# Kernel tuning notes

Hardware: AMD Instinct MI355X
Metric: run time of the kernel (lower is better)

## Reference

```python
import jax, jax.numpy as jnp
import numpy as np

D_MODEL = 256
NUM_HEADS = 4
HEAD_DIM = D_MODEL // NUM_HEADS


def setup_inputs() -> dict:
    key = jax.random.key(0)
    ks = jax.random.split(key, 16)
    B, N, M, C = 2, 256, 256, D_MODEL
    inp = {
        'q_tokens': jax.random.normal(ks[0], (B, N, C), jnp.float32),
        'k_tokens': jax.random.normal(ks[1], (B, M, C), jnp.float32),
        'v_tokens': jax.random.normal(ks[2], (B, M, C), jnp.float32),
        'qk_embeds': jax.random.normal(ks[3], (B, N, M, C), jnp.float32),
        'qv_embeds': jax.random.normal(ks[4], (B, N, M, C), jnp.float32),
    }
    scale = 1.0 / np.sqrt(C)
    # Linear layer params (weight used as x @ W + b)
    inp['Wq'] = jax.random.normal(ks[5], (C, C), jnp.float32) * scale
    inp['bq'] = jnp.zeros((C,), jnp.float32)
    inp['Wk'] = jax.random.normal(ks[6], (C, C), jnp.float32) * scale
    inp['bk'] = jnp.zeros((C,), jnp.float32)
    inp['Wv'] = jax.random.normal(ks[7], (C, C), jnp.float32) * scale
    inp['bv'] = jnp.zeros((C,), jnp.float32)
    inp['Wqk'] = jax.random.normal(ks[8], (C, C), jnp.float32) * scale
    inp['bqk'] = jnp.zeros((C,), jnp.float32)
    inp['Wqv'] = jax.random.normal(ks[9], (C, C), jnp.float32) * scale
    inp['bqv'] = jnp.zeros((C,), jnp.float32)
    return inp


def reference(q_tokens, k_tokens, v_tokens, qk_embeds, qv_embeds,
              Wq, bq, Wk, bk, Wv, bv, Wqk, bqk, Wqv, bqv):
    B, N, C = q_tokens.shape
    M = k_tokens.shape[1]
    H, hc = NUM_HEADS, HEAD_DIM

    # token projections -> (B, H, len, hc)
    q = (q_tokens @ Wq + bq).reshape(B, N, H, hc).transpose(0, 2, 1, 3)
    k = (k_tokens @ Wk + bk).reshape(B, M, H, hc).transpose(0, 2, 1, 3)
    v = (v_tokens @ Wv + bv).reshape(B, M, H, hc).transpose(0, 2, 1, 3)

    # pair-embedding projections -> (B, N, M, H, hc)
    qk = (qk_embeds @ Wqk + bqk).reshape(B, N, M, H, hc)
    qv = (qv_embeds @ Wqv + bqv).reshape(B, N, M, H, hc)

    # scores: q . (k + qk)  == q.k + q.qk
    scores = jnp.einsum('bhnc,bhmc->bhnm', q, k)
    scores = scores + jnp.einsum('bhnc,bnmhc->bhnm', q, qk)
    scores = scores / np.sqrt(hc).astype(np.float32)

    attn = jax.nn.softmax(scores, axis=-1)  # (B, H, N, M)

    # output: attn @ (v + qv) == attn@v + attn.qv
    hidden = jnp.einsum('bhnm,bhmc->bhnc', attn, v)
    hidden = hidden + jnp.einsum('bhnm,bnmhc->bhnc', attn, qv)
    hidden = hidden.transpose(0, 2, 1, 3).reshape(B, N, C)  # (B, N, C)
    return hidden, attn
```

## Files before the change

kernel.cpp:

```cpp
#include <hip/hip_runtime.h>

#define BB 2
#define NN 256
#define CC 256

__device__ __forceinline__ float dot4acc(float4 e, float4 w, float s) {
    s = fmaf(e.x, w.x, s); s = fmaf(e.y, w.y, s);
    s = fmaf(e.z, w.z, s); s = fmaf(e.w, w.w, s);
    return s;
}

__global__ __launch_bounds__(256) void proj_gemm(
    const float* __restrict__ q_tok, const float* __restrict__ k_tok, const float* __restrict__ v_tok,
    const float* __restrict__ Wq, const float* __restrict__ bq,
    const float* __restrict__ Wk, const float* __restrict__ bk,
    const float* __restrict__ Wv, const float* __restrict__ bv,
    float* __restrict__ out)
{
    const int row0 = blockIdx.x * 64;
    const int col0 = blockIdx.y * 64;
    const int seg  = row0 >> 9;
    const float* A    = seg == 0 ? q_tok : (seg == 1 ? k_tok : v_tok);
    const float* W    = seg == 0 ? Wq    : (seg == 1 ? Wk    : Wv);
    const float* bias = seg == 0 ? bq    : (seg == 1 ? bk    : bv);
    const int ar0 = row0 & 511;

    __shared__ float As[64][17];
    __shared__ float Bs[16][68];
    const int t  = threadIdx.x;
    const int tr = t >> 4, tc = t & 15;
    float acc[4][4] = {};

    const int sr  = t >> 2, sk4 = (t & 3) << 2;
    const int bkr = t >> 4, bj4 = (t & 15) << 2;

    for (int k0 = 0; k0 < 256; k0 += 16) {
        float4 a4 = *reinterpret_cast<const float4*>(&A[(ar0 + sr) * 256 + k0 + sk4]);
        float4 b4 = *reinterpret_cast<const float4*>(&W[(k0 + bkr) * 256 + col0 + bj4]);
        As[sr][sk4 + 0] = a4.x; As[sr][sk4 + 1] = a4.y; As[sr][sk4 + 2] = a4.z; As[sr][sk4 + 3] = a4.w;
        Bs[bkr][bj4 + 0] = b4.x; Bs[bkr][bj4 + 1] = b4.y; Bs[bkr][bj4 + 2] = b4.z; Bs[bkr][bj4 + 3] = b4.w;
        __syncthreads();
        #pragma unroll
        for (int k = 0; k < 16; ++k) {
            float a[4], bbv[4];
            #pragma unroll
            for (int i = 0; i < 4; ++i) a[i] = As[tr * 4 + i][k];
            #pragma unroll
            for (int j = 0; j < 4; ++j) bbv[j] = Bs[k][tc * 4 + j];
            #pragma unroll
            for (int i = 0; i < 4; ++i)
                #pragma unroll
                for (int j = 0; j < 4; ++j)
                    acc[i][j] = fmaf(a[i], bbv[j], acc[i][j]);
        }
        __syncthreads();
    }
    #pragma unroll
    for (int i = 0; i < 4; ++i) {
        const int r = row0 + tr * 4 + i;
        #pragma unroll
        for (int j = 0; j < 4; ++j) {
            const int cj = col0 + tc * 4 + j;
            out[r * 256 + cj] = acc[i][j] + bias[cj];
        }
    }
}

__global__ __launch_bounds__(256) void qw_gemm(
    const float* __restrict__ qp, const float* __restrict__ Wqk, float* __restrict__ qW)
{
    const int h    = blockIdx.z;
    const int row0 = blockIdx.x * 64;
    const int d0   = blockIdx.y * 64;
    __shared__ float As[64][17];
    __shared__ float Bs[16][68];
    const int t  = threadIdx.x;
    const int tr = t >> 4, tc = t & 15;
    float acc[4][4] = {};
    const int sr = t >> 2, sc4 = (t & 3) << 2;

    for (int k0 = 0; k0 < 64; k0 += 16) {
        float4 a4 = *reinterpret_cast<const float4*>(&qp[(row0 + sr) * 256 + h * 64 + k0 + sc4]);
        float4 b4 = *reinterpret_cast<const float4*>(&Wqk[(d0 + sr) * 256 + h * 64 + k0 + sc4]);
        As[sr][sc4 + 0] = a4.x; As[sr][sc4 + 1] = a4.y; As[sr][sc4 + 2] = a4.z; As[sr][sc4 + 3] = a4.w;
        Bs[sc4 + 0][sr] = b4.x; Bs[sc4 + 1][sr] = b4.y; Bs[sc4 + 2][sr] = b4.z; Bs[sc4 + 3][sr] = b4.w;
        __syncthreads();
        #pragma unroll
        for (int k = 0; k < 16; ++k) {
            float a[4], bbv[4];
            #pragma unroll
            for (int i = 0; i < 4; ++i) a[i] = As[tr * 4 + i][k];
            #pragma unroll
            for (int j = 0; j < 4; ++j) bbv[j] = Bs[k][tc * 4 + j];
            #pragma unroll
            for (int i = 0; i < 4; ++i)
                #pragma unroll
                for (int j = 0; j < 4; ++j)
                    acc[i][j] = fmaf(a[i], bbv[j], acc[i][j]);
        }
        __syncthreads();
    }
    #pragma unroll
    for (int i = 0; i < 4; ++i)
        #pragma unroll
        for (int j = 0; j < 4; ++j)
            qW[((row0 + tr * 4 + i) * 4 + h) * 256 + d0 + tc * 4 + j] = acc[i][j];
}

__global__ __launch_bounds__(256) void qk_gemm(
    const float* __restrict__ qkvp, float* __restrict__ Sqk)
{
    const int bh = blockIdx.z;
    const int b  = bh >> 2, h = bh & 3;
    const int n0 = blockIdx.x * 64;
    const int m0 = blockIdx.y * 64;
    __shared__ float As[64][17];
    __shared__ float Bs[16][68];
    const int t  = threadIdx.x;
    const int tr = t >> 4, tc = t & 15;
    float acc[4][4] = {};
    const int sr = t >> 2, sc4 = (t & 3) << 2;

    for (int k0 = 0; k0 < 64; k0 += 16) {
        float4 a4 = *reinterpret_cast<const float4*>(&qkvp[(size_t)(b * 256 + n0 + sr) * 256 + h * 64 + k0 + sc4]);
        float4 b4 = *reinterpret_cast<const float4*>(&qkvp[(size_t)(512 + b * 256 + m0 + sr) * 256 + h * 64 + k0 + sc4]);
        As[sr][sc4 + 0] = a4.x; As[sr][sc4 + 1] = a4.y; As[sr][sc4 + 2] = a4.z; As[sr][sc4 + 3] = a4.w;
        Bs[sc4 + 0][sr] = b4.x; Bs[sc4 + 1][sr] = b4.y; Bs[sc4 + 2][sr] = b4.z; Bs[sc4 + 3][sr] = b4.w;
        __syncthreads();
        #pragma unroll
        for (int k = 0; k < 16; ++k) {
            float a[4], bbv[4];
            #pragma unroll
            for (int i = 0; i < 4; ++i) a[i] = As[tr * 4 + i][k];
            #pragma unroll
            for (int j = 0; j < 4; ++j) bbv[j] = Bs[k][tc * 4 + j];
            #pragma unroll
            for (int i = 0; i < 4; ++i)
                #pragma unroll
                for (int j = 0; j < 4; ++j)
                    acc[i][j] = fmaf(a[i], bbv[j], acc[i][j]);
        }
        __syncthreads();
    }
    #pragma unroll
    for (int i = 0; i < 4; ++i)
        #pragma unroll
        for (int j = 0; j < 4; ++j)
            Sqk[(size_t)((b * 4 + h) * 256 + n0 + tr * 4 + i) * 256 + m0 + tc * 4 + j] = acc[i][j];
}

__global__ __launch_bounds__(512, 4) void mega3(
    const float* __restrict__ qk_emb, const float* __restrict__ qv_emb,
    const float* __restrict__ qkvp, const float* __restrict__ qW,
    const float* __restrict__ Sqk, const float* __restrict__ Wqv,
    const float* __restrict__ bqv,
    float* __restrict__ attn_out, float* __restrict__ hidden)
{
    const int bn = blockIdx.x;
    const int b  = bn >> 8, n = bn & 255;
    const int t  = threadIdx.x;
    const int w  = t >> 6, l = t & 63;

    __shared__ float qWs[1024];
    __shared__ float SqkL[1024];
    __shared__ float Ssc[1024];
    __shared__ float attn_s[1024];
    __shared__ float Ap[4096];
    __shared__ float stage[16][256];
    __shared__ float pr[2][256];
    __shared__ float mxs[8][4], sums[8][4], scl[8][4];

    if (t < 256)
        *reinterpret_cast<float4*>(&qWs[t * 4]) =
            *reinterpret_cast<const float4*>(&qW[(size_t)bn * 1024 + t * 4]);
    __syncthreads();

    const int lq = l & 15, lr = l >> 4, li = l & 31;

    if (l < 32) {
        #pragma unroll
        for (int h = 0; h < 4; ++h)
            SqkL[h * 256 + w * 32 + li] =
                Sqk[(size_t)((b * 4 + h) * 256 + n) * 256 + w * 32 + li];
    }

    #pragma unroll
    for (int g = 0; g < 8; g += 2) {
        const int m0 = w * 32 + g * 4 + lr;
        const float* r0 = qk_emb + (size_t)(bn * 256 + m0) * 256 + lq * 4;
        const float* r1 = r0 + 1024;
        const float4 e00 = *reinterpret_cast<const float4*>(r0);
        const float4 e01 = *reinterpret_cast<const float4*>(r0 + 64);
        const float4 e02 = *reinterpret_cast<const float4*>(r0 + 128);
        const float4 e03 = *reinterpret_cast<const float4*>(r0 + 192);
        const float4 e10 = *reinterpret_cast<const float4*>(r1);
        const float4 e11 = *reinterpret_cast<const float4*>(r1 + 64);
        const float4 e12 = *reinterpret_cast<const float4*>(r1 + 128);
        const float4 e13 = *reinterpret_cast<const float4*>(r1 + 192);
        float p0[4], p1[4];
        #pragma unroll
        for (int hh = 0; hh < 4; ++hh) {
            const float4 w0 = *reinterpret_cast<const float4*>(&qWs[hh * 256 + lq * 4]);
            const float4 w1 = *reinterpret_cast<const float4*>(&qWs[hh * 256 + 64 + lq * 4]);
            const float4 w2 = *reinterpret_cast<const float4*>(&qWs[hh * 256 + 128 + lq * 4]);
            const float4 w3 = *reinterpret_cast<const float4*>(&qWs[hh * 256 + 192 + lq * 4]);
            float s0 = 0.f, s1 = 0.f;
            s0 = dot4acc(e00, w0, s0); s0 = dot4acc(e01, w1, s0);
            s0 = dot4acc(e02, w2, s0); s0 = dot4acc(e03, w3, s0);
            s1 = dot4acc(e10, w0, s1); s1 = dot4acc(e11, w1, s1);
            s1 = dot4acc(e12, w2, s1); s1 = dot4acc(e13, w3, s1);
            p0[hh] = s0; p1[hh] = s1;
        }
        #pragma unroll
        for (int hh = 0; hh < 4; ++hh) {
            p0[hh] += __shfl_xor(p0[hh], 1); p1[hh] += __shfl_xor(p1[hh], 1);
            p0[hh] += __shfl_xor(p0[hh], 2); p1[hh] += __shfl_xor(p1[hh], 2);
            p0[hh] += __shfl_xor(p0[hh], 4); p1[hh] += __shfl_xor(p1[hh], 4);
            p0[hh] += __shfl_xor(p0[hh], 8); p1[hh] += __shfl_xor(p1[hh], 8);
        }
        if (lq == 0) {
            #pragma unroll
            for (int hh = 0; hh < 4; ++hh) {
                Ssc[hh * 256 + m0]     = p0[hh];
                Ssc[hh * 256 + m0 + 4] = p1[hh];
            }
        }
    }

    float mxw[4], smw[4];
    #pragma unroll
    for (int h = 0; h < 4; ++h) {
        const float sc = (Ssc[h * 256 + w * 32 + li] + SqkL[h * 256 + w * 32 + li]) * 0.125f;
        float mx = sc;
        #pragma unroll
        for (int mask = 16; mask >= 1; mask >>= 1) mx = fmaxf(mx, __shfl_xor(mx, mask));
        const float e = __expf(sc - mx);
        attn_s[h * 256 + w * 32 + li] = e;
        float sm = e;
        #pragma unroll
        for (int mask = 16; mask >= 1; mask >>= 1) sm += __shfl_xor(sm, mask);
        mxw[h] = mx; smw[h] = sm;
    }
    if (l == 0) {
        #pragma unroll
        for (int h = 0; h < 4; ++h) { mxs[w][h] = mxw[h]; sums[w][h] = smw[h]; }
    }

    float4 acc[4];
    #pragma unroll
    for (int hh = 0; hh < 4; ++hh) acc[hh] = make_float4(0.f, 0.f, 0.f, 0.f);
    {
        const float* rb = qv_emb + (size_t)(bn * 256 + w * 32) * 256 + l * 4;
        #pragma unroll
        for (int mm = 0; mm < 32; mm += 8) {
            float4 e[8];
            #pragma unroll
            for (int r = 0; r < 8; ++r)
                e[r] = *reinterpret_cast<const float4*>(rb + (size_t)(mm + r) * 256);
            #pragma unroll
            for (int r = 0; r < 8; ++r) {
                #pragma unroll
                for (int hh = 0; hh < 4; ++hh) {
                    const float a = attn_s[hh * 256 + w * 32 + mm + r];
                    acc[hh].x = fmaf(a, e[r].x, acc[hh].x);
                    acc[hh].y = fmaf(a, e[r].y, acc[hh].y);
                    acc[hh].z = fmaf(a, e[r].z, acc[hh].z);
                    acc[hh].w = fmaf(a, e[r].w, acc[hh].w);
                }
            }
        }
    }
    __syncthreads();

    if (t < 4) {
        const int h = t;
        float mg = mxs[0][h];
        #pragma unroll
        for (int ww = 1; ww < 8; ++ww) mg = fmaxf(mg, mxs[ww][h]);
        float sr[8]; float sg = 0.f;
        #pragma unroll
        for (int ww = 0; ww < 8; ++ww) { sr[ww] = __expf(mxs[ww][h] - mg); sg += sums[ww][h] * sr[ww]; }
        const float inv = 1.f / sg;
        #pragma unroll
        for (int ww = 0; ww < 8; ++ww) scl[ww][h] = sr[ww] * inv;
    }
    __syncthreads();

    {
        const int h = t >> 7, j = t & 127;
        float* ao = attn_out + (size_t)((b * 4 + h) * 256 + n) * 256;
        #pragma unroll
        for (int rep = 0; rep < 2; ++rep) {
            const int jj = j + rep * 128;
            const float a = attn_s[h * 256 + jj] * scl[jj >> 5][h];
            attn_s[h * 256 + jj] = a;
            ao[jj] = a;
        }
    }
    if (w < 4) {
        #pragma unroll
        for (int hh = 0; hh < 4; ++hh) {
            const float s = scl[w][hh];
            float4 v = acc[hh];
            v.x *= s; v.y *= s; v.z *= s; v.w *= s;
            *reinterpret_cast<float4*>(&Ap[(w * 4 + hh) * 256 + l * 4]) = v;
        }
    }
    __syncthreads();
    if (w >= 4) {
        #pragma unroll
        for (int hh = 0; hh < 4; ++hh) {
            const float s = scl[w][hh];
            float4* p = reinterpret_cast<float4*>(&Ap[((w - 4) * 4 + hh) * 256 + l * 4]);
            float4 o = *p;
            o.x = fmaf(acc[hh].x, s, o.x); o.y = fmaf(acc[hh].y, s, o.y);
            o.z = fmaf(acc[hh].z, s, o.z); o.w = fmaf(acc[hh].w, s, o.w);
            *p = o;
        }
    }
    __syncthreads();
    #pragma unroll
    for (int i = 0; i < 2; ++i) {
        const int idx = t + i * 512;
        const int hh = idx >> 8, d = idx & 255;
        Ap[hh * 256 + d] = Ap[hh * 256 + d] + Ap[(4 + hh) * 256 + d]
                         + Ap[(8 + hh) * 256 + d] + Ap[(12 + hh) * 256 + d];
    }

    {
        const int c = t & 255, half = t >> 8, hc = c >> 6;
        const int fr0 = t >> 6, fc0 = (t & 63) * 4;
        const int fr1 = fr0 + 8;
        const float* vbase = qkvp + (size_t)(1024 + b * 256) * 256;
        float4 ra = *reinterpret_cast<const float4*>(&vbase[(size_t)fr0 * 256 + fc0]);
        float4 rb = *reinterpret_cast<const float4*>(&vbase[(size_t)fr1 * 256 + fc0]);
        float hv = 0.f;
        for (int mt = 0; mt < 16; ++mt) {
            __syncthreads();
            *reinterpret_cast<float4*>(&stage[fr0][fc0]) = ra;
            *reinterpret_cast<float4*>(&stage[fr1][fc0]) = rb;
            if (mt < 15) {
                ra = *reinterpret_cast<const float4*>(&vbase[(size_t)((mt + 1) * 16 + fr0) * 256 + fc0]);
                rb = *reinterpret_cast<const float4*>(&vbase[(size_t)((mt + 1) * 16 + fr1) * 256 + fc0]);
            } else {
                ra = *reinterpret_cast<const float4*>(&Wqv[(size_t)fr0 * 256 + fc0]);
                rb = *reinterpret_cast<const float4*>(&Wqv[(size_t)fr1 * 256 + fc0]);
            }
            __syncthreads();
            #pragma unroll
            for (int r = 0; r < 8; ++r)
                hv = fmaf(attn_s[hc * 256 + mt * 16 + half * 8 + r], stage[half * 8 + r][c], hv);
        }
        for (int dt = 0; dt < 16; ++dt) {
            __syncthreads();
            *reinterpret_cast<float4*>(&stage[fr0][fc0]) = ra;
            *reinterpret_cast<float4*>(&stage[fr1][fc0]) = rb;
            if (dt < 15) {
                ra = *reinterpret_cast<const float4*>(&Wqv[(size_t)((dt + 1) * 16 + fr0) * 256 + fc0]);
                rb = *reinterpret_cast<const float4*>(&Wqv[(size_t)((dt + 1) * 16 + fr1) * 256 + fc0]);
            }
            __syncthreads();
            #pragma unroll
            for (int r = 0; r < 8; ++r)
                hv = fmaf(Ap[hc * 256 + dt * 16 + half * 8 + r], stage[half * 8 + r][c], hv);
        }
        pr[half][c] = hv;
    }
    __syncthreads();
    if (t < 256)
        hidden[(size_t)bn * 256 + t] = pr[0][t] + pr[1][t] + bqv[t];
}

extern "C" void kernel_launch(void* const* d_in, const int* in_sizes, int n_in,
                              void* d_out, int out_size, void* d_ws, size_t ws_size,
                              hipStream_t stream) {
    (void)in_sizes; (void)n_in; (void)out_size; (void)ws_size;
    const float* q_tok  = (const float*)d_in[0];
    const float* k_tok  = (const float*)d_in[1];
    const float* v_tok  = (const float*)d_in[2];
    const float* qk_emb = (const float*)d_in[3];
    const float* qv_emb = (const float*)d_in[4];
    const float* Wq  = (const float*)d_in[5];   const float* bq  = (const float*)d_in[6];
    const float* Wk  = (const float*)d_in[7];   const float* bk  = (const float*)d_in[8];
    const float* Wv  = (const float*)d_in[9];   const float* bv  = (const float*)d_in[10];
    const float* Wqk = (const float*)d_in[11];
    const float* Wqv = (const float*)d_in[13];  const float* bqv = (const float*)d_in[14];

    float* ws   = (float*)d_ws;
    float* qkvp = ws;
    float* qW   = ws + 393216;
    float* Sqk  = ws + 917504;

    float* hidden = (float*)d_out;
    float* attn   = (float*)d_out + BB * NN * CC;

    proj_gemm<<<dim3(24, 4),   256, 0, stream>>>(q_tok, k_tok, v_tok, Wq, bq, Wk, bk, Wv, bv, qkvp);
    qw_gemm  <<<dim3(8, 4, 4), 256, 0, stream>>>(qkvp, Wqk, qW);
    qk_gemm  <<<dim3(4, 4, 8), 256, 0, stream>>>(qkvp, Sqk);
    mega3    <<<512,           512, 0, stream>>>(qk_emb, qv_emb, qkvp, qW, Sqk, Wqv, bqv, attn, hidden);
}
```

Baseline: 92.13 us.

## Stream pair-embedding tiles into LDS with double-buffered global_load_lds in fused kernel

Result: no change. 93.41 us (+1.4%).

```diff
diff --git a/kernel.cpp b/kernel.cpp
--- a/kernel.cpp
+++ b/kernel.cpp
@@ -9,6 +9,18 @@
     s = fmaf(e.z, w.z, s); s = fmaf(e.w, w.w, s);
     return s;
 }
+
+#define GLL(gaddr, laddr)                                                     \
+    __builtin_amdgcn_global_load_lds(                                         \
+        (const __attribute__((address_space(1))) void*)(gaddr),               \
+        (__attribute__((address_space(3))) void*)(laddr), 16, 0, 0)
+
+#define STAGE_TILE(B, SRCBASE, TT)                                            \
+    do {                                                                      \
+        const float* _g = (SRCBASE) + (size_t)(TT) * 4096;                    \
+        GLL(_g + (w * 2) * 256 + l * 4,     (B) + (w * 2) * 256);             \
+        GLL(_g + (w * 2 + 1) * 256 + l * 4, (B) + (w * 2 + 1) * 256);         \
+    } while (0)
 
 __global__ __launch_bounds__(256) void proj_gemm(
     const float* __restrict__ q_tok, const float* __restrict__ k_tok, const float* __restrict__ v_tok,
@@ -149,7 +161,7 @@
             Sqk[(size_t)((b * 4 + h) * 256 + n0 + tr * 4 + i) * 256 + m0 + tc * 4 + j] = acc[i][j];
 }
 
-__global__ __launch_bounds__(512, 4) void mega3(
+__global__ __launch_bounds__(512, 4) void mega6(
     const float* __restrict__ qk_emb, const float* __restrict__ qv_emb,
     const float* __restrict__ qkvp, const float* __restrict__ qW,
     const float* __restrict__ Sqk, const float* __restrict__ Wqv,
@@ -161,160 +173,157 @@
     const int t  = threadIdx.x;
     const int w  = t >> 6, l = t & 63;
 
-    __shared__ float qWs[1024];
-    __shared__ float SqkL[1024];
-    __shared__ float Ssc[1024];
-    __shared__ float attn_s[1024];
-    __shared__ float Ap[4096];
-    __shared__ float stage[16][256];
-    __shared__ float pr[2][256];
-    __shared__ float mxs[8][4], sums[8][4], scl[8][4];
-
-    if (t < 256)
-        *reinterpret_cast<float4*>(&qWs[t * 4]) =
-            *reinterpret_cast<const float4*>(&qW[(size_t)bn * 1024 + t * 4]);
-    __syncthreads();
-
-    const int lq = l & 15, lr = l >> 4, li = l & 31;
-
-    if (l < 32) {
-        #pragma unroll
-        for (int h = 0; h < 4; ++h)
-            SqkL[h * 256 + w * 32 + li] =
-                Sqk[(size_t)((b * 4 + h) * 256 + n) * 256 + w * 32 + li];
-    }
-
-    #pragma unroll
-    for (int g = 0; g < 8; g += 2) {
-        const int m0 = w * 32 + g * 4 + lr;
-        const float* r0 = qk_emb + (size_t)(bn * 256 + m0) * 256 + lq * 4;
-        const float* r1 = r0 + 1024;
-        const float4 e00 = *reinterpret_cast<const float4*>(r0);
-        const float4 e01 = *reinterpret_cast<const float4*>(r0 + 64);
-        const float4 e02 = *reinterpret_cast<const float4*>(r0 + 128);
-        const float4 e03 = *reinterpret_cast<const float4*>(r0 + 192);
-        const float4 e10 = *reinterpret_cast<const float4*>(r1);
-        const float4 e11 = *reinterpret_cast<const float4*>(r1 + 64);
-        const float4 e12 = *reinterpret_cast<const float4*>(r1 + 128);
-        const float4 e13 = *reinterpret_cast<const float4*>(r1 + 192);
-        float p0[4], p1[4];
-        #pragma unroll
-        for (int hh = 0; hh < 4; ++hh) {
-            const float4 w0 = *reinterpret_cast<const float4*>(&qWs[hh * 256 + lq * 4]);
-            const float4 w1 = *reinterpret_cast<const float4*>(&qWs[hh * 256 + 64 + lq * 4]);
-            const float4 w2 = *reinterpret_cast<const float4*>(&qWs[hh * 256 + 128 + lq * 4]);
-            const float4 w3 = *reinterpret_cast<const float4*>(&qWs[hh * 256 + 192 + lq * 4]);
-            float s0 = 0.f, s1 = 0.f;
-            s0 = dot4acc(e00, w0, s0); s0 = dot4acc(e01, w1, s0);
-            s0 = dot4acc(e02, w2, s0); s0 = dot4acc(e03, w3, s0);
-            s1 = dot4acc(e10, w0, s1); s1 = dot4acc(e11, w1, s1);
-            s1 = dot4acc(e12, w2, s1); s1 = dot4acc(e13, w3, s1);
-            p0[hh] = s0; p1[hh] = s1;
-        }
-        #pragma unroll
-        for (int hh = 0; hh < 4; ++hh) {
-            p0[hh] += __shfl_xor(p0[hh], 1); p1[hh] += __shfl_xor(p1[hh], 1);
-            p0[hh] += __shfl_xor(p0[hh], 2); p1[hh] += __shfl_xor(p1[hh], 2);
-            p0[hh] += __shfl_xor(p0[hh], 4); p1[hh] += __shfl_xor(p1[hh], 4);
-            p0[hh] += __shfl_xor(p0[hh], 8); p1[hh] += __shfl_xor(p1[hh], 8);
-        }
-        if (lq == 0) {
-            #pragma unroll
-            for (int hh = 0; hh < 4; ++hh) {
-                Ssc[hh * 256 + m0]     = p0[hh];
-                Ssc[hh * 256 + m0 + 4] = p1[hh];
-            }
-        }
-    }
-
-    float mxw[4], smw[4];
-    #pragma unroll
-    for (int h = 0; h < 4; ++h) {
-        const float sc = (Ssc[h * 256 + w * 32 + li] + SqkL[h * 256 + w * 32 + li]) * 0.125f;
-        float mx = sc;
-        #pragma unroll
-        for (int mask = 16; mask >= 1; mask >>= 1) mx = fmaxf(mx, __shfl_xor(mx, mask));
-        const float e = __expf(sc - mx);
-        attn_s[h * 256 + w * 32 + li] = e;
-        float sm = e;
-        #pragma unroll
-        for (int mask = 16; mask >= 1; mask >>= 1) sm += __shfl_xor(sm, mask);
-        mxw[h] = mx; smw[h] = sm;
-    }
-    if (l == 0) {
-        #pragma unroll
-        for (int h = 0; h < 4; ++h) { mxs[w][h] = mxw[h]; sums[w][h] = smw[h]; }
-    }
-
-    float4 acc[4];
-    #pragma unroll
-    for (int hh = 0; hh < 4; ++hh) acc[hh] = make_float4(0.f, 0.f, 0.f, 0.f);
+    __shared__ __align__(16) float buf0[4096];
+    __shared__ __align__(16) float buf1[4096];
+    __shared__ __align__(16) float qWs[1024];
+    __shared__ __align__(16) float SqkL[1024];
+    __shared__ __align__(16) float Ssc[1024];
+    __shared__ __align__(16) float attn_s[1024];
+    __shared__ __align__(16) float Ap[4096];
+    __shared__ __align__(16) float pr[2][256];
+    __shared__ float mxs[8][4], sums[8][4];
+
+    const float* qkb = qk_emb + (size_t)bn * 65536;
+    const float* qvb = qv_emb + (size_t)bn * 65536;
+
+    STAGE_TILE(buf0, qkb, 0);
     {
-        const float* rb = qv_emb + (size_t)(bn * 256 + w * 32) * 256 + l * 4;
-        #pragma unroll
-        for (int mm = 0; mm < 32; mm += 8) {
-            float4 e[8];
-            #pragma unroll
-            for (int r = 0; r < 8; ++r)
-                e[r] = *reinterpret_cast<const float4*>(rb + (size_t)(mm + r) * 256);
-            #pragma unroll
-            for (int r = 0; r < 8; ++r) {
-                #pragma unroll
-                for (int hh = 0; hh < 4; ++hh) {
-                    const float a = attn_s[hh * 256 + w * 32 + mm + r];
-                    acc[hh].x = fmaf(a, e[r].x, acc[hh].x);
-                    acc[hh].y = fmaf(a, e[r].y, acc[hh].y);
-                    acc[hh].z = fmaf(a, e[r].z, acc[hh].z);
-                    acc[hh].w = fmaf(a, e[r].w, acc[hh].w);
-                }
-            }
-        }
-    }
-    __syncthreads();
-
-    if (t < 4) {
-        const int h = t;
-        float mg = mxs[0][h];
-        #pragma unroll
-        for (int ww = 1; ww < 8; ++ww) mg = fmaxf(mg, mxs[ww][h]);
-        float sr[8]; float sg = 0.f;
-        #pragma unroll
-        for (int ww = 0; ww < 8; ++ww) { sr[ww] = __expf(mxs[ww][h] - mg); sg += sums[ww][h] * sr[ww]; }
-        const float inv = 1.f / sg;
-        #pragma unroll
-        for (int ww = 0; ww < 8; ++ww) scl[ww][h] = sr[ww] * inv;
-    }
-    __syncthreads();
-
+        const int i2 = t * 2;
+        *reinterpret_cast<float2*>(&qWs[i2]) =
+            *reinterpret_cast<const float2*>(&qW[(size_t)bn * 1024 + i2]);
+        const int h = i2 >> 8, m = i2 & 255;
+        *reinterpret_cast<float2*>(&SqkL[i2]) =
+            *reinterpret_cast<const float2*>(&Sqk[(size_t)((b * 4 + h) * 256 + n) * 256 + m]);
+    }
+    __syncthreads();
+
+    const int rl  = l >> 5;
+    const int sub = l & 31;
+    const int lq  = sub & 15;
+    const int hp  = sub >> 4;
+    const int rloc = w * 2 + rl;
+    const int h0 = hp * 2, h1 = hp * 2 + 1;
+
+    float4 qr0[4], qr1[4];
+    #pragma unroll
+    for (int c = 0; c < 4; ++c) {
+        qr0[c] = *reinterpret_cast<const float4*>(&qWs[h0 * 256 + c * 64 + lq * 4]);
+        qr1[c] = *reinterpret_cast<const float4*>(&qWs[h1 * 256 + c * 64 + lq * 4]);
+    }
+
+    for (int tt = 0; tt < 16; ++tt) {
+        float* cur = (tt & 1) ? buf1 : buf0;
+        float* nxt = (tt & 1) ? buf0 : buf1;
+        if (tt < 15) STAGE_TILE(nxt, qkb, tt + 1);
+
+        const float* er = cur + rloc * 256 + lq * 4;
+        const float4 e0 = *reinterpret_cast<const float4*>(er);
+        const float4 e1 = *reinterpret_cast<const float4*>(er + 64);
+        const float4 e2 = *reinterpret_cast<const float4*>(er + 128);
+        const float4 e3 = *reinterpret_cast<const float4*>(er + 192);
+        float s0 = 0.f, s1 = 0.f;
+        s0 = dot4acc(e0, qr0[0], s0); s0 = dot4acc(e1, qr0[1], s0);
+        s0 = dot4acc(e2, qr0[2], s0); s0 = dot4acc(e3, qr0[3], s0);
+        s1 = dot4acc(e0, qr1[0], s1); s1 = dot4acc(e1, qr1[1], s1);
+        s1 = dot4acc(e2, qr1[2], s1); s1 = dot4acc(e3, qr1[3], s1);
+        s0 += __shfl_xor(s0, 1); s1 += __shfl_xor(s1, 1);
+        s0 += __shfl_xor(s0, 2); s1 += __shfl_xor(s1, 2);
+        s0 += __shfl_xor(s0, 4); s1 += __shfl_xor(s1, 4);
+        s0 += __shfl_xor(s0, 8); s1 += __shfl_xor(s1, 8);
+        if ((l & 15) == 0) {
+            const int m = tt * 16 + rloc;
+            Ssc[h0 * 256 + m] = s0;
+            Ssc[h1 * 256 + m] = s1;
+        }
+        __syncthreads();
+    }
+
+    STAGE_TILE(buf0, qvb, 0);
+
+    const int li = l & 31;
     {
-        const int h = t >> 7, j = t & 127;
-        float* ao = attn_out + (size_t)((b * 4 + h) * 256 + n) * 256;
+        float mxw[4], smw[4];
+        #pragma unroll
+        for (int h = 0; h < 4; ++h) {
+            const float sc = (Ssc[h * 256 + w * 32 + li] + SqkL[h * 256 + w * 32 + li]) * 0.125f;
+            float mx = sc;
+            #pragma unroll
+            for (int mask = 16; mask >= 1; mask >>= 1) mx = fmaxf(mx, __shfl_xor(mx, mask));
+            const float e = __expf(sc - mx);
+            if (l < 32) attn_s[h * 256 + w * 32 + li] = e;
+            float sm = e;
+            #pragma unroll
+            for (int mask = 16; mask >= 1; mask >>= 1) sm += __shfl_xor(sm, mask);
+            mxw[h] = mx; smw[h] = sm;
+        }
+        if (l == 0) {
+            #pragma unroll
+            for (int h = 0; h < 4; ++h) { mxs[w][h] = mxw[h]; sums[w][h] = smw[h]; }
+        }
+    }
+    __syncthreads();
+
+    {
+        float mgv[4], invv[4];
+        #pragma unroll
+        for (int h = 0; h < 4; ++h) {
+            float mg = mxs[0][h];
+            #pragma unroll
+            for (int ww = 1; ww < 8; ++ww) mg = fmaxf(mg, mxs[ww][h]);
+            float sg = 0.f;
+            #pragma unroll
+            for (int ww = 0; ww < 8; ++ww) sg += sums[ww][h] * __expf(mxs[ww][h] - mg);
+            mgv[h] = mg; invv[h] = 1.f / sg;
+        }
+        const int h2 = t >> 7, j = t & 127;
+        float* ao = attn_out + (size_t)((b * 4 + h2) * 256 + n) * 256;
         #pragma unroll
         for (int rep = 0; rep < 2; ++rep) {
             const int jj = j + rep * 128;
-            const float a = attn_s[h * 256 + jj] * scl[jj >> 5][h];
-            attn_s[h * 256 + jj] = a;
+            const float s = __expf(mxs[jj >> 5][h2] - mgv[h2]) * invv[h2];
+            const float a = attn_s[h2 * 256 + jj] * s;
+            attn_s[h2 * 256 + jj] = a;
             ao[jj] = a;
         }
     }
+    __syncthreads();
+
+    float4 acc[4];
+    #pragma unroll
+    for (int hh = 0; hh < 4; ++hh) acc[hh] = make_float4(0.f, 0.f, 0.f, 0.f);
+
+    for (int tt = 0; tt < 16; ++tt) {
+        float* cur = (tt & 1) ? buf1 : buf0;
+        float* nxt = (tt & 1) ? buf0 : buf1;
+        if (tt < 15) STAGE_TILE(nxt, qvb, tt + 1);
+
+        const int m0 = tt * 16 + w * 2;
+        const float4 e0 = *reinterpret_cast<const float4*>(&cur[(w * 2) * 256 + l * 4]);
+        const float4 e1 = *reinterpret_cast<const float4*>(&cur[(w * 2 + 1) * 256 + l * 4]);
+        #pragma unroll
+        for (int hh = 0; hh < 4; ++hh) {
+            const float a0 = attn_s[hh * 256 + m0];
+            const float a1 = attn_s[hh * 256 + m0 + 1];
+            acc[hh].x = fmaf(a0, e0.x, acc[hh].x); acc[hh].y = fmaf(a0, e0.y, acc[hh].y);
+            acc[hh].z = fmaf(a0, e0.z, acc[hh].z); acc[hh].w = fmaf(a0, e0.w, acc[hh].w);
+            acc[hh].x = fmaf(a1, e1.x, acc[hh].x); acc[hh].y = fmaf(a1, e1.y, acc[hh].y);
+            acc[hh].z = fmaf(a1, e1.z, acc[hh].z); acc[hh].w = fmaf(a1, e1.w, acc[hh].w);
+        }
+        __syncthreads();
+    }
+
     if (w < 4) {
         #pragma unroll
+        for (int hh = 0; hh < 4; ++hh)
+            *reinterpret_cast<float4*>(&Ap[(w * 4 + hh) * 256 + l * 4]) = acc[hh];
+    }
+    __syncthreads();
+    if (w >= 4) {
+        #pragma unroll
         for (int hh = 0; hh < 4; ++hh) {
-            const float s = scl[w][hh];
-            float4 v = acc[hh];
-            v.x *= s; v.y *= s; v.z *= s; v.w *= s;
-            *reinterpret_cast<float4*>(&Ap[(w * 4 + hh) * 256 + l * 4]) = v;
-        }
-    }
-    __syncthreads();
-    if (w >= 4) {
-        #pragma unroll
-        for (int hh = 0; hh < 4; ++hh) {
-            const float s = scl[w][hh];
             float4* p = reinterpret_cast<float4*>(&Ap[((w - 4) * 4 + hh) * 256 + l * 4]);
             float4 o = *p;
-            o.x = fmaf(acc[hh].x, s, o.x); o.y = fmaf(acc[hh].y, s, o.y);
-            o.z = fmaf(acc[hh].z, s, o.z); o.w = fmaf(acc[hh].w, s, o.w);
+            o.x += acc[hh].x; o.y += acc[hh].y; o.z += acc[hh].z; o.w += acc[hh].w;
             *p = o;
         }
     }
@@ -328,6 +337,7 @@
     }
 
     {
+        float* stg = buf0;
         const int c = t & 255, half = t >> 8, hc = c >> 6;
         const int fr0 = t >> 6, fc0 = (t & 63) * 4;
         const int fr1 = fr0 + 8;
@@ -337,8 +347,8 @@
         float hv = 0.f;
         for (int mt = 0; mt < 16; ++mt) {
             __syncthreads();
-            *reinterpret_cast<float4*>(&stage[fr0][fc0]) = ra;
-            *reinterpret_cast<float4*>(&stage[fr1][fc0]) = rb;
+            *reinterpret_cast<float4*>(&stg[fr0 * 256 + fc0]) = ra;
+            *reinterpret_cast<float4*>(&stg[fr1 * 256 + fc0]) = rb;
             if (mt < 15) {
                 ra = *reinterpret_cast<const float4*>(&vbase[(size_t)((mt + 1) * 16 + fr0) * 256 + fc0]);
                 rb = *reinterpret_cast<const float4*>(&vbase[(size_t)((mt + 1) * 16 + fr1) * 256 + fc0]);
@@ -349,12 +359,12 @@
             __syncthreads();
             #pragma unroll
             for (int r = 0; r < 8; ++r)
-                hv = fmaf(attn_s[hc * 256 + mt * 16 + half * 8 + r], stage[half * 8 + r][c], hv);
+                hv = fmaf(attn_s[hc * 256 + mt * 16 + half * 8 + r], stg[(half * 8 + r) * 256 + c], hv);
         }
         for (int dt = 0; dt < 16; ++dt) {
             __syncthreads();
-            *reinterpret_cast<float4*>(&stage[fr0][fc0]) = ra;
-            *reinterpret_cast<float4*>(&stage[fr1][fc0]) = rb;
+            *reinterpret_cast<float4*>(&stg[fr0 * 256 + fc0]) = ra;
+            *reinterpret_cast<float4*>(&stg[fr1 * 256 + fc0]) = rb;
             if (dt < 15) {
                 ra = *reinterpret_cast<const float4*>(&Wqv[(size_t)((dt + 1) * 16 + fr0) * 256 + fc0]);
                 rb = *reinterpret_cast<const float4*>(&Wqv[(size_t)((dt + 1) * 16 + fr1) * 256 + fc0]);
@@ -362,7 +372,7 @@
             __syncthreads();
             #pragma unroll
             for (int r = 0; r < 8; ++r)
-                hv = fmaf(Ap[hc * 256 + dt * 16 + half * 8 + r], stage[half * 8 + r][c], hv);
+                hv = fmaf(Ap[hc * 256 + dt * 16 + half * 8 + r], stg[(half * 8 + r) * 256 + c], hv);
         }
         pr[half][c] = hv;
     }
@@ -397,5 +407,5 @@
     proj_gemm<<<dim3(24, 4),   256, 0, stream>>>(q_tok, k_tok, v_tok, Wq, bq, Wk, bk, Wv, bv, qkvp);
     qw_gemm  <<<dim3(8, 4, 4), 256, 0, stream>>>(qkvp, Wqk, qW);
     qk_gemm  <<<dim3(4, 4, 8), 256, 0, stream>>>(qkvp, Sqk);
-    mega3    <<<512,           512, 0, stream>>>(qk_emb, qv_emb, qkvp, qW, Sqk, Wqv, bqv, attn, hidden);
-}
+    mega6    <<<512,           512, 0, stream>>>(qk_emb, qv_emb, qkvp, qW, Sqk, Wqv, bqv, attn, hidden);
+}
```
